# Optimization experiments

Measured on AMD Instinct MI355X. Metric: run time of the kernel, lower is better.

The kernel has to match this reference:

```python
import jax, jax.numpy as jnp
import numpy as np

N = 200_000   # hits
K = 512       # truth objects (showers)
D = 3         # clustering-space dim
Q_MIN = 1.0
REPULSION_CONTRIB = 0.5


def _oc_loss(coords, truth_indices):
    """Object-condensation attractive/repulsive loss (LLClusterCoordinates,
    3-input branch: beta fixed at 0.5, use_average_cc_pos=1, Q_MIN=1, S_B=0)."""
    n = coords.shape[0]
    tidx = truth_indices[:, 0]
    notnoise = (tidx >= 0).astype(coords.dtype)           # [N]
    seg = jnp.clip(tidx, 0, K - 1)                        # safe segment ids

    # beta_like = 0.5 everywhere -> charge q_i = arctanh(beta)^2 + Q_MIN
    beta = jnp.full((n,), 0.5, dtype=coords.dtype)
    q = jnp.arctanh(beta) ** 2 + Q_MIN                    # [N]

    # per-object condensation charge from max-beta hit
    beta_max = jax.ops.segment_max(jnp.where(tidx >= 0, beta, 0.0), seg, num_segments=K)
    obj_present = jax.ops.segment_sum(notnoise, seg, num_segments=K) > 0
    q_alpha = jnp.arctanh(jnp.clip(beta_max, 0.0, 1.0 - 1e-4)) ** 2 + Q_MIN
    q_alpha = jnp.where(obj_present, q_alpha, 0.0)        # [K] (absent objs contribute 0)

    # q-weighted average condensation-point position (use_average_cc_pos = 1.0)
    w = q * notnoise                                      # [N]
    wsum = jax.ops.segment_sum(w, seg, num_segments=K)    # [K]
    cc = jax.ops.segment_sum(coords * w[:, None], seg, num_segments=K) \
         / jnp.maximum(wsum, 1e-6)[:, None]               # [K, D]

    # pairwise squared distances hit -> condensation point  [N, K]
    d2 = jnp.sum((coords[:, None, :] - cc[None, :, :]) ** 2, axis=-1)

    # attractive: each non-noise hit pulled to its own object's cc (squared dist)
    d2_own = jnp.take_along_axis(d2, seg[:, None], axis=1)[:, 0]      # [N]
    qa_own = q_alpha[seg]                                             # [N]
    V_att = jnp.sum(q * qa_own * d2_own * notnoise) / n

    # repulsive hinge: every hit pushed from every OTHER object's cc
    d = jnp.sqrt(d2 + 1e-6)
    rep_all = jnp.sum(q_alpha[None, :] * jax.nn.relu(1.0 - d), axis=1)          # [N]
    d_own = jnp.sqrt(d2_own + 1e-6)
    rep_own = qa_own * jax.nn.relu(1.0 - d_own) * notnoise                      # [N]
    V_rep = jnp.sum(q * (rep_all - rep_own)) / n

    return (1.0 - REPULSION_CONTRIB) * V_att + REPULSION_CONTRIB * V_rep


def setup_inputs() -> dict:
    key = jax.random.key(0)
    k1, k2 = jax.random.split(key)
    coords = jax.random.normal(k1, (N, D), dtype=jnp.float32)
    truth_indices = jax.random.randint(k2, (N, 1), 0, K).astype(jnp.int32)
    row_splits = jnp.array([0, N], dtype=jnp.int32)
    return {"coords": coords, "truth_indices": truth_indices, "row_splits": row_splits}


def reference(coords, truth_indices, row_splits):
    # single event: row_splits == [0, N]; loss is per-event so segments suffice
    return _oc_loss(coords, truth_indices)
```

## Files before the change

kernel.cpp:

```cpp
#include <hip/hip_runtime.h>
#include <math.h>

#define K_CLUSTERS 512
#define QCONST 1.3017372f


__global__ __launch_bounds__(256) void oc_bins_kernel(
    const float* __restrict__ coords, const int* __restrict__ tidx,
    float* __restrict__ bins, int n) {
    __shared__ float sb[K_CLUSTERS * 4];
    for (int j = threadIdx.x; j < K_CLUSTERS * 4; j += blockDim.x) sb[j] = 0.0f;
    __syncthreads();
    for (int i = blockIdx.x * blockDim.x + threadIdx.x; i < n;
         i += gridDim.x * blockDim.x) {
        int t = tidx[i];
        if (t >= 0) {
            int seg = t < K_CLUSTERS ? t : K_CLUSTERS - 1;
            float x = coords[3 * i + 0];
            float y = coords[3 * i + 1];
            float z = coords[3 * i + 2];
            atomicAdd(&sb[4 * seg + 0], QCONST);
            atomicAdd(&sb[4 * seg + 1], QCONST * x);
            atomicAdd(&sb[4 * seg + 2], QCONST * y);
            atomicAdd(&sb[4 * seg + 3], QCONST * z);
        }
    }
    __syncthreads();
    for (int j = threadIdx.x; j < K_CLUSTERS * 4; j += blockDim.x) {
        float v = sb[j];
        if (v != 0.0f) atomicAdd(&bins[j], v);
    }
}

__global__ void oc_cc_kernel(float* __restrict__ ws, float* __restrict__ out) {
    int k = threadIdx.x + blockIdx.x * blockDim.x;
    if (k == 0) *out = 0.0f;
    if (k < K_CLUSTERS) {
        float w  = ws[4 * k + 0];
        float wx = ws[4 * k + 1];
        float wy = ws[4 * k + 2];
        float wz = ws[4 * k + 3];
        float inv = 1.0f / fmaxf(w, 1e-6f);
        float qa = (w > 0.0f) ? QCONST : 0.0f;
        float4 c = make_float4(wx * inv, wy * inv, wz * inv, qa);
        reinterpret_cast<float4*>(ws + 4 * K_CLUSTERS)[k] = c;
    }
}

__global__ __launch_bounds__(256) void oc_main_kernel(
    const float* __restrict__ coords, const int* __restrict__ tidx,
    const float4* __restrict__ ccq, float* __restrict__ out, int n) {
    __shared__ float4 sc[K_CLUSTERS];
    for (int j = threadIdx.x; j < K_CLUSTERS; j += blockDim.x) sc[j] = ccq[j];
    __syncthreads();

    int i = blockIdx.x * blockDim.x + threadIdx.x;
    float contrib = 0.0f;
    if (i < n) {
        float x = coords[3 * i + 0];
        float y = coords[3 * i + 1];
        float z = coords[3 * i + 2];
        int t = tidx[i];
        float notnoise = (t >= 0) ? 1.0f : 0.0f;
        int seg = (t < 0) ? 0 : (t < K_CLUSTERS ? t : K_CLUSTERS - 1);

        float rep_all = 0.0f;
        #pragma unroll 8
        for (int k = 0; k < K_CLUSTERS; ++k) {
            float4 c = sc[k];
            float dx = x - c.x, dy = y - c.y, dz = z - c.z;
            float de = fmaf(dx, dx, 1e-6f);
            de = fmaf(dy, dy, de);
            de = fmaf(dz, dz, de);
            float d = __builtin_amdgcn_sqrtf(de);
            float tt = fmaxf(1.0f - d, 0.0f);
            rep_all = fmaf(c.w, tt, rep_all);
        }
        float4 co = sc[seg];
        float dx = x - co.x, dy = y - co.y, dz = z - co.z;
        float d2own = fmaf(dx, dx, fmaf(dy, dy, dz * dz));
        float down = __builtin_amdgcn_sqrtf(d2own + 1e-6f);
        float rep_own = co.w * fmaxf(1.0f - down, 0.0f) * notnoise;
        float att = QCONST * co.w * d2own * notnoise;
        float rep = QCONST * (rep_all - rep_own);
        contrib = 0.5f * att + 0.5f * rep;
    }

    #pragma unroll
    for (int off = 32; off > 0; off >>= 1)
        contrib += __shfl_down(contrib, off, 64);
    __shared__ float wpart[4];
    int wid = threadIdx.x >> 6;
    int lane = threadIdx.x & 63;
    if (lane == 0) wpart[wid] = contrib;
    __syncthreads();
    if (threadIdx.x == 0) {
        float s = wpart[0] + wpart[1] + wpart[2] + wpart[3];
        atomicAdd(out, s * (1.0f / (float)n));
    }
}

extern "C" void kernel_launch(void* const* d_in, const int* in_sizes, int n_in,
                              void* d_out, int out_size, void* d_ws, size_t ws_size,
                              hipStream_t stream) {
    const float* coords = (const float*)d_in[0];
    const int* tidx = (const int*)d_in[1];
    int n = in_sizes[1];
    float* ws = (float*)d_ws;
    float* out = (float*)d_out;

    hipMemsetAsync(ws, 0, K_CLUSTERS * 4 * sizeof(float), stream);
    oc_bins_kernel<<<128, 256, 0, stream>>>(coords, tidx, ws, n);
    oc_cc_kernel<<<1, K_CLUSTERS, 0, stream>>>(ws, out);
    int blocks = (n + 255) / 256;
    oc_main_kernel<<<blocks, 256, 0, stream>>>(
        coords, tidx, (const float4*)(ws + 4 * K_CLUSTERS), out, n);
}
```

Before: 110.1 us.

## Expand distances algebraically, fuse centroid kernel, process two hits per thread

The centroid kernel is folded into the main kernel's shared-memory preload, and the output zeroing moves into the binning kernel, which removes one launch. Each stored centroid entry becomes (-2c, |c|^2), so the squared distance costs three FMAs plus the hit's own norm. The repulsive sum relu(1-d) is rewritten as K - sum(min(d,1)), with constants moved into one final scale; absent clusters get a huge |c|^2 so they add nothing. Each thread now handles two hits so every shared-memory centroid read serves both. The costs are halved block count and the precision risk of the expanded-distance form.

Measured after the change: 102.3 us. 7.0% less time.

```diff
diff --git a/kernel.cpp b/kernel.cpp
--- a/kernel.cpp
+++ b/kernel.cpp
@@ -1,90 +1,95 @@
 #include <hip/hip_runtime.h>
 #include <math.h>
 
-#define K_CLUSTERS 512
-#define QCONST 1.3017372f
+#define K_CL 512
+#define QC 1.3017372f
 
 
-__global__ __launch_bounds__(256) void oc_bins_kernel(
+__global__ __launch_bounds__(256) void oc_bins(
     const float* __restrict__ coords, const int* __restrict__ tidx,
-    float* __restrict__ bins, int n) {
-    __shared__ float sb[K_CLUSTERS * 4];
-    for (int j = threadIdx.x; j < K_CLUSTERS * 4; j += blockDim.x) sb[j] = 0.0f;
+    float* __restrict__ bins, float* __restrict__ out, int n) {
+    __shared__ float sb[K_CL * 4];
+    for (int j = threadIdx.x; j < K_CL * 4; j += 256) sb[j] = 0.0f;
+    if (blockIdx.x == 0 && threadIdx.x == 0) *out = 0.0f;
     __syncthreads();
-    for (int i = blockIdx.x * blockDim.x + threadIdx.x; i < n;
-         i += gridDim.x * blockDim.x) {
+    int stride = gridDim.x * 256;
+    for (int i = blockIdx.x * 256 + threadIdx.x; i < n; i += stride) {
         int t = tidx[i];
         if (t >= 0) {
-            int seg = t < K_CLUSTERS ? t : K_CLUSTERS - 1;
+            int seg = t < K_CL ? t : K_CL - 1;
             float x = coords[3 * i + 0];
             float y = coords[3 * i + 1];
             float z = coords[3 * i + 2];
-            atomicAdd(&sb[4 * seg + 0], QCONST);
-            atomicAdd(&sb[4 * seg + 1], QCONST * x);
-            atomicAdd(&sb[4 * seg + 2], QCONST * y);
-            atomicAdd(&sb[4 * seg + 3], QCONST * z);
+            atomicAdd(&sb[4 * seg + 0], QC);
+            atomicAdd(&sb[4 * seg + 1], QC * x);
+            atomicAdd(&sb[4 * seg + 2], QC * y);
+            atomicAdd(&sb[4 * seg + 3], QC * z);
         }
     }
     __syncthreads();
-    for (int j = threadIdx.x; j < K_CLUSTERS * 4; j += blockDim.x) {
+    for (int j = threadIdx.x; j < K_CL * 4; j += 256) {
         float v = sb[j];
-        if (v != 0.0f) atomicAdd(&bins[j], v);
+        if (v != 0.0f) unsafeAtomicAdd(&bins[j], v);
     }
 }
 
-__global__ void oc_cc_kernel(float* __restrict__ ws, float* __restrict__ out) {
-    int k = threadIdx.x + blockIdx.x * blockDim.x;
-    if (k == 0) *out = 0.0f;
-    if (k < K_CLUSTERS) {
-        float w  = ws[4 * k + 0];
-        float wx = ws[4 * k + 1];
-        float wy = ws[4 * k + 2];
-        float wz = ws[4 * k + 3];
+__global__ __launch_bounds__(256) void oc_main(
+    const float* __restrict__ coords, const int* __restrict__ tidx,
+    const float4* __restrict__ bins4, float* __restrict__ out,
+    int n, int half, float scale) {
+    __shared__ float4 sa[K_CL];
+    for (int k = threadIdx.x; k < K_CL; k += 256) {
+        float4 b = bins4[k];
+        float w = b.x;
         float inv = 1.0f / fmaxf(w, 1e-6f);
-        float qa = (w > 0.0f) ? QCONST : 0.0f;
-        float4 c = make_float4(wx * inv, wy * inv, wz * inv, qa);
-        reinterpret_cast<float4*>(ws + 4 * K_CLUSTERS)[k] = c;
+        float cx = b.y * inv, cy = b.z * inv, cz = b.w * inv;
+        float c2 = cx * cx + cy * cy + cz * cz;
+        sa[k] = (w > 0.0f) ? make_float4(-2.0f * cx, -2.0f * cy, -2.0f * cz, c2)
+                           : make_float4(0.0f, 0.0f, 0.0f, 1e30f);
     }
-}
-
-__global__ __launch_bounds__(256) void oc_main_kernel(
-    const float* __restrict__ coords, const int* __restrict__ tidx,
-    const float4* __restrict__ ccq, float* __restrict__ out, int n) {
-    __shared__ float4 sc[K_CLUSTERS];
-    for (int j = threadIdx.x; j < K_CLUSTERS; j += blockDim.x) sc[j] = ccq[j];
     __syncthreads();
 
-    int i = blockIdx.x * blockDim.x + threadIdx.x;
-    float contrib = 0.0f;
-    if (i < n) {
-        float x = coords[3 * i + 0];
-        float y = coords[3 * i + 1];
-        float z = coords[3 * i + 2];
-        int t = tidx[i];
-        float notnoise = (t >= 0) ? 1.0f : 0.0f;
-        int seg = (t < 0) ? 0 : (t < K_CLUSTERS ? t : K_CLUSTERS - 1);
+    int g = blockIdx.x * 256 + threadIdx.x;
+    int i1 = g, i2 = g + half;
+    bool v1 = i1 < half;
+    bool v2 = i2 < n;
 
-        float rep_all = 0.0f;
-        #pragma unroll 8
-        for (int k = 0; k < K_CLUSTERS; ++k) {
-            float4 c = sc[k];
-            float dx = x - c.x, dy = y - c.y, dz = z - c.z;
-            float de = fmaf(dx, dx, 1e-6f);
-            de = fmaf(dy, dy, de);
-            de = fmaf(dz, dz, de);
-            float d = __builtin_amdgcn_sqrtf(de);
-            float tt = fmaxf(1.0f - d, 0.0f);
-            rep_all = fmaf(c.w, tt, rep_all);
-        }
-        float4 co = sc[seg];
-        float dx = x - co.x, dy = y - co.y, dz = z - co.z;
-        float d2own = fmaf(dx, dx, fmaf(dy, dy, dz * dz));
-        float down = __builtin_amdgcn_sqrtf(d2own + 1e-6f);
-        float rep_own = co.w * fmaxf(1.0f - down, 0.0f) * notnoise;
-        float att = QCONST * co.w * d2own * notnoise;
-        float rep = QCONST * (rep_all - rep_own);
-        contrib = 0.5f * att + 0.5f * rep;
+    float x1 = 0.f, y1 = 0.f, z1 = 0.f; int t1 = -1;
+    float x2 = 0.f, y2 = 0.f, z2 = 0.f; int t2 = -1;
+    if (v1) { x1 = coords[3*i1]; y1 = coords[3*i1+1]; z1 = coords[3*i1+2]; t1 = tidx[i1]; }
+    if (v2) { x2 = coords[3*i2]; y2 = coords[3*i2+1]; z2 = coords[3*i2+2]; t2 = tidx[i2]; }
+
+    float sp1 = fmaf(x1, x1, fmaf(y1, y1, z1 * z1));
+    float sp2 = fmaf(x2, x2, fmaf(y2, y2, z2 * z2));
+    float se1 = sp1 + 1e-6f;
+    float se2 = sp2 + 1e-6f;
+
+    float r1 = 0.0f, r2 = 0.0f;
+    #pragma unroll 4
+    for (int k = 0; k < K_CL; ++k) {
+        float4 a = sa[k];
+        float e1 = fmaf(x1, a.x, fmaf(y1, a.y, fmaf(z1, a.z, se1 + a.w)));
+        float e2 = fmaf(x2, a.x, fmaf(y2, a.y, fmaf(z2, a.z, se2 + a.w)));
+        float d1 = __builtin_amdgcn_sqrtf(e1);
+        float d2 = __builtin_amdgcn_sqrtf(e2);
+        r1 += fminf(d1, 1.0f);
+        r2 += fminf(d2, 1.0f);
     }
+
+    float nn1 = (t1 >= 0) ? 1.0f : 0.0f;
+    float nn2 = (t2 >= 0) ? 1.0f : 0.0f;
+    int s1 = (t1 < 0) ? 0 : (t1 < K_CL ? t1 : K_CL - 1);
+    int s2 = (t2 < 0) ? 0 : (t2 < K_CL ? t2 : K_CL - 1);
+    float4 o1 = sa[s1];
+    float4 o2 = sa[s2];
+    float d2o1 = fmaxf(sp1 + o1.w + fmaf(x1, o1.x, fmaf(y1, o1.y, z1 * o1.z)), 0.0f);
+    float d2o2 = fmaxf(sp2 + o2.w + fmaf(x2, o2.x, fmaf(y2, o2.y, z2 * o2.z)), 0.0f);
+    float tto1 = fmaxf(1.0f - __builtin_amdgcn_sqrtf(d2o1 + 1e-6f), 0.0f);
+    float tto2 = fmaxf(1.0f - __builtin_amdgcn_sqrtf(d2o2 + 1e-6f), 0.0f);
+
+    float c1 = nn1 * (d2o1 - tto1) + ((float)K_CL - r1);
+    float c2 = nn2 * (d2o2 - tto2) + ((float)K_CL - r2);
+    float contrib = (v1 ? c1 : 0.0f) + (v2 ? c2 : 0.0f);
 
     #pragma unroll
     for (int off = 32; off > 0; off >>= 1)
@@ -96,7 +101,7 @@
     __syncthreads();
     if (threadIdx.x == 0) {
         float s = wpart[0] + wpart[1] + wpart[2] + wpart[3];
-        atomicAdd(out, s * (1.0f / (float)n));
+        unsafeAtomicAdd(out, s * scale);
     }
 }
 
@@ -109,10 +114,12 @@
     float* ws = (float*)d_ws;
     float* out = (float*)d_out;
 
-    hipMemsetAsync(ws, 0, K_CLUSTERS * 4 * sizeof(float), stream);
-    oc_bins_kernel<<<128, 256, 0, stream>>>(coords, tidx, ws, n);
-    oc_cc_kernel<<<1, K_CLUSTERS, 0, stream>>>(ws, out);
-    int blocks = (n + 255) / 256;
-    oc_main_kernel<<<blocks, 256, 0, stream>>>(
-        coords, tidx, (const float4*)(ws + 4 * K_CLUSTERS), out, n);
+    hipMemsetAsync(ws, 0, K_CL * 4 * sizeof(float), stream);
+    oc_bins<<<128, 256, 0, stream>>>(coords, tidx, ws, out, n);
+
+    int half = (n + 1) / 2;
+    int blocks = (half + 255) / 256;
+    float scale = 0.5f * QC * QC / (float)n;
+    oc_main<<<blocks, 256, 0, stream>>>(
+        coords, tidx, (const float4*)ws, out, n, half, scale);
 }
```
